# Optimization experiments

Measured on AMD Instinct MI355X. Metric: run time of the kernel, lower is better.

## Reference

```python
import jax, jax.numpy as jnp
import numpy as np

B, L, D_IN, D_H, D_OUT = 8, 1024, 1024, 1024, 1024


def setup_inputs() -> dict:
    key = jax.random.key(0)
    ks = jax.random.split(key, 9)
    s = 0.02  # weight scale to keep ReLU chain stable
    return {
        "leaves": jax.random.normal(ks[0], (B, L, D_IN), dtype=jnp.float32),
        "V_w": jax.random.normal(ks[1], (D_H, D_IN), dtype=jnp.float32) * s,
        "V_b": jax.random.normal(ks[2], (D_H,), dtype=jnp.float32) * s,
        "U_w": jax.random.normal(ks[3], (D_H, D_H), dtype=jnp.float32) * s,
        "U_b": jax.random.normal(ks[4], (D_H,), dtype=jnp.float32) * s,
        "W_w": jax.random.normal(ks[5], (D_H, D_H), dtype=jnp.float32) * s,
        "W_b": jax.random.normal(ks[6], (D_H,), dtype=jnp.float32) * s,
        "O_w": jax.random.normal(ks[7], (D_OUT, D_H), dtype=jnp.float32) * s,
        "O_b": jax.random.normal(ks[8], (D_OUT,), dtype=jnp.float32) * s,
    }


def reference(leaves, V_w, V_b, U_w, U_b, W_w, W_b, O_w, O_b):
    # Leaf encoding: h_leaf = relu(V(x))            [B, L, H]
    h = jax.nn.relu(jnp.einsum("bli,hi->blh", leaves, V_w) + V_b)
    # Depth-batched recursion over the complete binary tree:
    # combined = relu(U(left) + W(right)); log2(L) levels, node count halves.
    while h.shape[1] > 1:
        left, right = h[:, 0::2], h[:, 1::2]  # [B, n/2, H] each
        h = jax.nn.relu(
            jnp.einsum("bnh,gh->bng", left, U_w) + U_b
            + jnp.einsum("bnh,gh->bng", right, W_w) + W_b
        )
    root = h[:, 0]  # [B, H]
    logits = jnp.einsum("bh,oh->bo", root, O_w) + O_b
    return jax.nn.log_softmax(logits, axis=-1)
```

## Files before the change

### kernel.cpp

```cpp
#include <hip/hip_runtime.h>
#include <hip/hip_bf16.h>
#include <math.h>

typedef __bf16 bf16_t;
typedef __bf16 bf16x8 __attribute__((ext_vector_type(8)));
typedef __bf16 bf16x4 __attribute__((ext_vector_type(4)));
typedef float  f32x4  __attribute__((ext_vector_type(4)));

#define GLD_LDS16(g, l)                                                          \
  __builtin_amdgcn_global_load_lds((const __attribute__((address_space(1))) void*)(g), \
                                   (__attribute__((address_space(3))) void*)(l), 16, 0, 0)

__global__ __launch_bounds__(256) void k_cvt_bf16(const float* __restrict__ in,
                                                  bf16_t* __restrict__ out, int n4) {
  int i = blockIdx.x * 256 + threadIdx.x;
  if (i >= n4) return;
  float4 v = reinterpret_cast<const float4*>(in)[i];
  bf16x4 o;
  o[0] = (bf16_t)v.x; o[1] = (bf16_t)v.y; o[2] = (bf16_t)v.z; o[3] = (bf16_t)v.w;
  reinterpret_cast<bf16x4*>(out)[i] = o;
}

__global__ __launch_bounds__(256) void k_build_uw(const float* __restrict__ U,
                                                  const float* __restrict__ W,
                                                  const float* __restrict__ Ub,
                                                  const float* __restrict__ Wb,
                                                  bf16_t* __restrict__ UW,
                                                  float* __restrict__ buw) {
  int idx = blockIdx.x * 256 + threadIdx.x;
  int i = idx * 4;
  int g = i >> 11;
  int k = i & 2047;
  const float* src = (k < 1024) ? (U + g * 1024 + k) : (W + g * 1024 + (k - 1024));
  float4 v = *reinterpret_cast<const float4*>(src);
  bf16x4 o;
  o[0] = (bf16_t)v.x; o[1] = (bf16_t)v.y; o[2] = (bf16_t)v.z; o[3] = (bf16_t)v.w;
  reinterpret_cast<bf16x4*>(UW)[idx] = o;
  if (idx < 1024) buw[idx] = Ub[idx] + Wb[idx];
}

template <int TM, bool SPLIT>
__global__ __launch_bounds__(256) void k_gemm(const bf16_t* __restrict__ A,
                                              const bf16_t* __restrict__ Bw,
                                              const float* __restrict__ bias,
                                              bf16_t* __restrict__ C,
                                              float* __restrict__ P,
                                              int M, int K, int kchunk) {
  constexpr int N = 1024;
  constexpr int MI = TM / 32;
  __shared__ bf16_t As[3][TM * 32];
  __shared__ bf16_t Bs[3][128 * 32];

  const int tid = threadIdx.x;
  const int lane = tid & 63;
  const int wave = tid >> 6;
  const int wr = wave >> 1, wc = wave & 1;
  const int bm = blockIdx.x, bn = blockIdx.y, bz = blockIdx.z;
  const int kbase = bz * kchunk;

  const bf16_t* Abase = A + (size_t)bm * TM * K + kbase;
  const bf16_t* Bbase = Bw + (size_t)bn * 128 * K + kbase;

  f32x4 acc[MI][4] = {};
  const int rl = lane & 15, kq = lane >> 4;

  auto stage = [&](int buf, int ko) {
#pragma unroll
    for (int it = 0; it < TM / 64; ++it) {
      int c = tid + 256 * it;
      int r = c >> 2, kbp = c & 3;
      int kb = kbp ^ ((r >> 1) & 3);
      GLD_LDS16(Abase + (size_t)r * K + ko + kb * 8, &As[buf][c * 8]);
    }
#pragma unroll
    for (int it = 0; it < 2; ++it) {
      int c = tid + 256 * it;
      int r = c >> 2, kbp = c & 3;
      int kb = kbp ^ ((r >> 1) & 3);
      GLD_LDS16(Bbase + (size_t)r * K + ko + kb * 8, &Bs[buf][c * 8]);
    }
  };

  const int kiters = kchunk >> 5;
  stage(0, 0);
  stage(1, 32);

  int cur = 0;
  for (int t = 0; t < kiters; ++t) {
    if (t + 1 < kiters) {
      asm volatile("s_waitcnt vmcnt(3)" ::: "memory");
    } else {
      asm volatile("s_waitcnt vmcnt(0)" ::: "memory");
    }
    __builtin_amdgcn_s_barrier();
    __builtin_amdgcn_sched_barrier(0);
    if (t + 2 < kiters) {
      int b2 = cur + 2; if (b2 >= 3) b2 -= 3;
      stage(b2, (t + 2) * 32);
    }
    bf16x8 af[MI], bfr[4];
#pragma unroll
    for (int i = 0; i < MI; ++i) {
      int r = wr * (TM / 2) + i * 16 + rl;
      int kbp = kq ^ ((r >> 1) & 3);
      af[i] = *reinterpret_cast<const bf16x8*>(&As[cur][r * 32 + kbp * 8]);
    }
#pragma unroll
    for (int j = 0; j < 4; ++j) {
      int r = wc * 64 + j * 16 + rl;
      int kbp = kq ^ ((r >> 1) & 3);
      bfr[j] = *reinterpret_cast<const bf16x8*>(&Bs[cur][r * 32 + kbp * 8]);
    }
#pragma unroll
    for (int i = 0; i < MI; ++i)
#pragma unroll
      for (int j = 0; j < 4; ++j)
        acc[i][j] = __builtin_amdgcn_mfma_f32_16x16x32_bf16(af[i], bfr[j], acc[i][j], 0, 0, 0);
    if (++cur >= 3) cur = 0;
  }

  const int rq = lane >> 4, cl = lane & 15;
  if (SPLIT) {
    float* Pp = P + (size_t)bz * M * N;
#pragma unroll
    for (int i = 0; i < MI; ++i) {
#pragma unroll
      for (int j = 0; j < 4; ++j) {
        int grow = bm * TM + wr * (TM / 2) + i * 16 + rq * 4;
        int gcol = bn * 128 + wc * 64 + j * 16 + cl;
#pragma unroll
        for (int reg = 0; reg < 4; ++reg)
          Pp[(size_t)(grow + reg) * N + gcol] = acc[i][j][reg];
      }
    }
  } else {
#pragma unroll
    for (int j = 0; j < 4; ++j) {
      int gcol = bn * 128 + wc * 64 + j * 16 + cl;
      float bv = bias[gcol];
#pragma unroll
      for (int i = 0; i < MI; ++i) {
        int grow = bm * TM + wr * (TM / 2) + i * 16 + rq * 4;
#pragma unroll
        for (int reg = 0; reg < 4; ++reg) {
          float v = acc[i][j][reg] + bv;
          v = v > 0.0f ? v : 0.0f;
          C[(size_t)(grow + reg) * N + gcol] = (bf16_t)v;
        }
      }
    }
  }
}

__global__ __launch_bounds__(256) void k_reduce(const float* __restrict__ P,
                                                const float* __restrict__ bias,
                                                bf16_t* __restrict__ C, int M, int ks) {
  constexpr int N = 1024;
  int idx = blockIdx.x * 256 + threadIdx.x;
  int col = (idx * 4) & (N - 1);
  int row = (idx * 4) >> 10;
  float4 s = *reinterpret_cast<const float4*>(P + (size_t)row * N + col);
  for (int z = 1; z < ks; ++z) {
    float4 v = *reinterpret_cast<const float4*>(P + ((size_t)z * M + row) * N + col);
    s.x += v.x; s.y += v.y; s.z += v.z; s.w += v.w;
  }
  float4 b = *reinterpret_cast<const float4*>(bias + col);
  bf16x4 o;
  o[0] = (bf16_t)fmaxf(s.x + b.x, 0.0f);
  o[1] = (bf16_t)fmaxf(s.y + b.y, 0.0f);
  o[2] = (bf16_t)fmaxf(s.z + b.z, 0.0f);
  o[3] = (bf16_t)fmaxf(s.w + b.w, 0.0f);
  reinterpret_cast<bf16x4*>(C)[idx] = o;
}

__global__ __launch_bounds__(256) void k_tail(const bf16_t* __restrict__ A,
                                              const bf16_t* __restrict__ Bw,
                                              const float* __restrict__ bias,
                                              bf16_t* __restrict__ C, int M) {
  constexpr int N = 1024, K = 2048;
  const int lane = threadIdx.x & 63;
  const int gw = blockIdx.x * 4 + (threadIdx.x >> 6);
  const int n = gw & (N - 1);
  const int mbase = (gw >> 10) * 8;
  const int k0 = lane * 32;

  float bv[32];
  const bf16_t* bp = Bw + (size_t)n * K + k0;
#pragma unroll
  for (int q = 0; q < 4; ++q) {
    bf16x8 v = *reinterpret_cast<const bf16x8*>(bp + q * 8);
#pragma unroll
    for (int j = 0; j < 8; ++j) bv[q * 8 + j] = (float)v[j];
  }

  float acc[8];
#pragma unroll
  for (int m = 0; m < 8; ++m) {
    const bf16_t* ap = A + (size_t)(mbase + m) * K + k0;
    float s = 0.0f;
#pragma unroll
    for (int q = 0; q < 4; ++q) {
      bf16x8 v = *reinterpret_cast<const bf16x8*>(ap + q * 8);
#pragma unroll
      for (int j = 0; j < 8; ++j) s += (float)v[j] * bv[q * 8 + j];
    }
    acc[m] = s;
  }
#pragma unroll
  for (int m = 0; m < 8; ++m) {
    acc[m] += __shfl_xor(acc[m], 32, 64);
    acc[m] += __shfl_xor(acc[m], 16, 64);
    acc[m] += __shfl_xor(acc[m], 8, 64);
    acc[m] += __shfl_xor(acc[m], 4, 64);
    acc[m] += __shfl_xor(acc[m], 2, 64);
    acc[m] += __shfl_xor(acc[m], 1, 64);
  }
  if (lane < 8 && mbase + lane < M) {
    float v = acc[lane] + bias[n];
    v = v > 0.0f ? v : 0.0f;
    C[(size_t)(mbase + lane) * N + n] = (bf16_t)v;
  }
}

__global__ __launch_bounds__(256) void k_logits(const bf16_t* __restrict__ root,
                                                const bf16_t* __restrict__ Ow,
                                                const float* __restrict__ Ob,
                                                float* __restrict__ out) {
  int o = blockIdx.x * 256 + threadIdx.x;
  int b = blockIdx.y;
  const bf16_t* r = root + b * 1024;
  const bf16_t* w = Ow + (size_t)o * 1024;
  float s = 0.0f;
#pragma unroll 4
  for (int k = 0; k < 1024; k += 8) {
    bf16x8 rv = *reinterpret_cast<const bf16x8*>(r + k);
    bf16x8 wv = *reinterpret_cast<const bf16x8*>(w + k);
#pragma unroll
    for (int j = 0; j < 8; ++j) s += (float)rv[j] * (float)wv[j];
  }
  out[b * 1024 + o] = s + Ob[o];
}

__device__ inline float wave_max_f(float v) {
#pragma unroll
  for (int off = 32; off > 0; off >>= 1) v = fmaxf(v, __shfl_xor(v, off, 64));
  return v;
}
__device__ inline float wave_sum_f(float v) {
#pragma unroll
  for (int off = 32; off > 0; off >>= 1) v += __shfl_xor(v, off, 64);
  return v;
}

__global__ __launch_bounds__(256) void k_logsoftmax(const float* __restrict__ logits,
                                                    float* __restrict__ out) {
  int b = blockIdx.x;
  const float* x = logits + b * 1024;
  int tid = threadIdx.x;
  int wave = tid >> 6, lane = tid & 63;
  __shared__ float red[8];

  float m = -1e30f;
  for (int i = tid; i < 1024; i += 256) m = fmaxf(m, x[i]);
  m = wave_max_f(m);
  if (lane == 0) red[wave] = m;
  __syncthreads();
  if (tid == 0) red[4] = fmaxf(fmaxf(red[0], red[1]), fmaxf(red[2], red[3]));
  __syncthreads();
  m = red[4];

  float s = 0.0f;
  for (int i = tid; i < 1024; i += 256) s += expf(x[i] - m);
  s = wave_sum_f(s);
  if (lane == 0) red[wave] = s;
  __syncthreads();
  if (tid == 0) red[5] = logf(red[0] + red[1] + red[2] + red[3]);
  __syncthreads();
  float lse = m + red[5];
  for (int i = tid; i < 1024; i += 256) out[b * 1024 + i] = x[i] - lse;
}

extern "C" void kernel_launch(void* const* d_in, const int* in_sizes, int n_in,
                              void* d_out, int out_size, void* d_ws, size_t ws_size,
                              hipStream_t stream) {
  const float* leaves = (const float*)d_in[0];
  const float* V_w = (const float*)d_in[1];
  const float* V_b = (const float*)d_in[2];
  const float* U_w = (const float*)d_in[3];
  const float* U_b = (const float*)d_in[4];
  const float* W_w = (const float*)d_in[5];
  const float* W_b = (const float*)d_in[6];
  const float* O_w = (const float*)d_in[7];
  const float* O_b = (const float*)d_in[8];
  float* out = (float*)d_out;

  char* ws = (char*)d_ws;
  size_t off = 0;
  auto alloc = [&](size_t bytes) -> void* {
    off = (off + 255) & ~(size_t)255;
    void* p = ws + off;
    off += bytes;
    return p;
  };

  const size_t MB16 = (size_t)8192 * 1024 * 2;
  bf16_t* leaves_bf = (bf16_t*)alloc(MB16);
  bf16_t* Vw_bf = (bf16_t*)alloc((size_t)1024 * 1024 * 2);
  bf16_t* UW_bf = (bf16_t*)alloc((size_t)2 * 1024 * 1024 * 2);
  bf16_t* Ow_bf = (bf16_t*)alloc((size_t)1024 * 1024 * 2);
  float* buw = (float*)alloc(1024 * 4);
  bf16_t* hA = (bf16_t*)alloc(MB16);
  float* logits = (float*)alloc(8 * 1024 * 4);
  float* Pbuf = (float*)alloc((size_t)4 * 2048 * 1024 * 4);
  (void)ws_size; (void)in_sizes; (void)n_in; (void)out_size;

  k_cvt_bf16<<<(8 * 1024 * 1024 / 4) / 256, 256, 0, stream>>>(leaves, leaves_bf, 8 * 1024 * 1024 / 4);
  k_cvt_bf16<<<(1024 * 1024 / 4) / 256, 256, 0, stream>>>(V_w, Vw_bf, 1024 * 1024 / 4);
  k_cvt_bf16<<<(1024 * 1024 / 4) / 256, 256, 0, stream>>>(O_w, Ow_bf, 1024 * 1024 / 4);
  k_build_uw<<<2048, 256, 0, stream>>>(U_w, W_w, U_b, W_b, UW_bf, buw);

  k_gemm<64, false><<<dim3(128, 8), 256, 0, stream>>>(leaves_bf, Vw_bf, V_b, hA, nullptr,
                                                      8192, 1024, 1024);

  bf16_t* src = hA;
  bf16_t* dst = leaves_bf;
  auto swap = [&]() { bf16_t* t = src; src = dst; dst = t; };

  k_gemm<64, false><<<dim3(64, 8), 256, 0, stream>>>(src, UW_bf, buw, dst, nullptr,
                                                     4096, 2048, 2048);
  swap();
  k_gemm<64, true><<<dim3(32, 8, 2), 256, 0, stream>>>(src, UW_bf, nullptr, nullptr, Pbuf,
                                                       2048, 2048, 1024);
  k_reduce<<<2048 * 1024 / 4 / 256, 256, 0, stream>>>(Pbuf, buw, dst, 2048, 2);
  swap();
  k_gemm<64, true><<<dim3(16, 8, 4), 256, 0, stream>>>(src, UW_bf, nullptr, nullptr, Pbuf,
                                                       1024, 2048, 512);
  k_reduce<<<1024 * 1024 / 4 / 256, 256, 0, stream>>>(Pbuf, buw, dst, 1024, 4);
  swap();
  k_gemm<64, true><<<dim3(8, 8, 4), 256, 0, stream>>>(src, UW_bf, nullptr, nullptr, Pbuf,
                                                      512, 2048, 512);
  k_reduce<<<512 * 1024 / 4 / 256, 256, 0, stream>>>(Pbuf, buw, dst, 512, 4);
  swap();
  k_gemm<64, true><<<dim3(4, 8, 8), 256, 0, stream>>>(src, UW_bf, nullptr, nullptr, Pbuf,
                                                      256, 2048, 256);
  k_reduce<<<256 * 1024 / 4 / 256, 256, 0, stream>>>(Pbuf, buw, dst, 256, 8);
  swap();
  k_gemm<64, true><<<dim3(2, 8, 8), 256, 0, stream>>>(src, UW_bf, nullptr, nullptr, Pbuf,
                                                      128, 2048, 256);
  k_reduce<<<128 * 1024 / 4 / 256, 256, 0, stream>>>(Pbuf, buw, dst, 128, 8);
  swap();
  for (int M = 64; M >= 8; M >>= 1) {
    int blocks = (M / 8) * 1024 / 4;
    k_tail<<<blocks, 256, 0, stream>>>(src, UW_bf, buw, dst, M);
    swap();
  }

  k_logits<<<dim3(4, 8), 256, 0, stream>>>(src, Ow_bf, O_b, logits);
  k_logsoftmax<<<8, 256, 0, stream>>>(logits, out);
}
```

Measured before the change: 233.7 us.

## Replace split-K GEMM plus reduce with narrower-N tiles; fuse conversion kernels

Merges the four fp32-to-bf16 conversion launches into one grid-stride kernel. For tree levels M=2048..128, drops the split-K GEMM that wrote fp32 partials and the separate reduce kernel. These levels now use a single full-K GEMM with a 64x64 tile, which doubles the N-dimension block count and fuses bias+ReLU into the epilogue. This removes the partial-sum round trip through memory and one launch per level. The cost is fewer blocks on the small levels, with each block running the full K=2048 loop serially, so the late levels may lose parallelism.

```diff
diff --git a/kernel.cpp b/kernel.cpp
--- a/kernel.cpp
+++ b/kernel.cpp
@@ -11,57 +11,69 @@
   __builtin_amdgcn_global_load_lds((const __attribute__((address_space(1))) void*)(g), \
                                    (__attribute__((address_space(3))) void*)(l), 16, 0, 0)
 
-__global__ __launch_bounds__(256) void k_cvt_bf16(const float* __restrict__ in,
-                                                  bf16_t* __restrict__ out, int n4) {
-  int i = blockIdx.x * 256 + threadIdx.x;
-  if (i >= n4) return;
-  float4 v = reinterpret_cast<const float4*>(in)[i];
-  bf16x4 o;
-  o[0] = (bf16_t)v.x; o[1] = (bf16_t)v.y; o[2] = (bf16_t)v.z; o[3] = (bf16_t)v.w;
-  reinterpret_cast<bf16x4*>(out)[i] = o;
-}
-
-__global__ __launch_bounds__(256) void k_build_uw(const float* __restrict__ U,
-                                                  const float* __restrict__ W,
-                                                  const float* __restrict__ Ub,
-                                                  const float* __restrict__ Wb,
-                                                  bf16_t* __restrict__ UW,
-                                                  float* __restrict__ buw) {
-  int idx = blockIdx.x * 256 + threadIdx.x;
-  int i = idx * 4;
-  int g = i >> 11;
-  int k = i & 2047;
-  const float* src = (k < 1024) ? (U + g * 1024 + k) : (W + g * 1024 + (k - 1024));
-  float4 v = *reinterpret_cast<const float4*>(src);
-  bf16x4 o;
-  o[0] = (bf16_t)v.x; o[1] = (bf16_t)v.y; o[2] = (bf16_t)v.z; o[3] = (bf16_t)v.w;
-  reinterpret_cast<bf16x4*>(UW)[idx] = o;
-  if (idx < 1024) buw[idx] = Ub[idx] + Wb[idx];
-}
-
-template <int TM, bool SPLIT>
-__global__ __launch_bounds__(256) void k_gemm(const bf16_t* __restrict__ A,
-                                              const bf16_t* __restrict__ Bw,
-                                              const float* __restrict__ bias,
-                                              bf16_t* __restrict__ C,
-                                              float* __restrict__ P,
-                                              int M, int K, int kchunk) {
-  constexpr int N = 1024;
+__global__ __launch_bounds__(256) void k_cvt_all(const float* __restrict__ leaves,
+                                                 const float* __restrict__ V_w,
+                                                 const float* __restrict__ O_w,
+                                                 const float* __restrict__ U_w,
+                                                 const float* __restrict__ W_w,
+                                                 const float* __restrict__ U_b,
+                                                 const float* __restrict__ W_b,
+                                                 bf16_t* __restrict__ leaves_bf,
+                                                 bf16_t* __restrict__ Vw_bf,
+                                                 bf16_t* __restrict__ Ow_bf,
+                                                 bf16_t* __restrict__ UW_bf,
+                                                 float* __restrict__ buw) {
+  const int gtid = blockIdx.x * 256 + threadIdx.x;
+  const int G = gridDim.x * 256;
+  for (int i = gtid; i < 2097152; i += G) {
+    float4 v = reinterpret_cast<const float4*>(leaves)[i];
+    bf16x4 o; o[0] = (bf16_t)v.x; o[1] = (bf16_t)v.y; o[2] = (bf16_t)v.z; o[3] = (bf16_t)v.w;
+    reinterpret_cast<bf16x4*>(leaves_bf)[i] = o;
+  }
+  for (int i = gtid; i < 262144; i += G) {
+    float4 v = reinterpret_cast<const float4*>(V_w)[i];
+    bf16x4 o; o[0] = (bf16_t)v.x; o[1] = (bf16_t)v.y; o[2] = (bf16_t)v.z; o[3] = (bf16_t)v.w;
+    reinterpret_cast<bf16x4*>(Vw_bf)[i] = o;
+  }
+  for (int i = gtid; i < 262144; i += G) {
+    float4 v = reinterpret_cast<const float4*>(O_w)[i];
+    bf16x4 o; o[0] = (bf16_t)v.x; o[1] = (bf16_t)v.y; o[2] = (bf16_t)v.z; o[3] = (bf16_t)v.w;
+    reinterpret_cast<bf16x4*>(Ow_bf)[i] = o;
+  }
+  for (int idx = gtid; idx < 524288; idx += G) {
+    int i = idx * 4;
+    int g = i >> 11;
+    int k = i & 2047;
+    const float* src = (k < 1024) ? (U_w + g * 1024 + k) : (W_w + g * 1024 + (k - 1024));
+    float4 v = *reinterpret_cast<const float4*>(src);
+    bf16x4 o; o[0] = (bf16_t)v.x; o[1] = (bf16_t)v.y; o[2] = (bf16_t)v.z; o[3] = (bf16_t)v.w;
+    reinterpret_cast<bf16x4*>(UW_bf)[idx] = o;
+  }
+  if (gtid < 1024) buw[gtid] = U_b[gtid] + W_b[gtid];
+}
+
+template <int TM, int TN>
+__global__ __launch_bounds__(256, 4) void k_gemm(const bf16_t* __restrict__ A,
+                                                 const bf16_t* __restrict__ Bw,
+                                                 const float* __restrict__ bias,
+                                                 bf16_t* __restrict__ C,
+                                                 int K) {
   constexpr int MI = TM / 32;
+  constexpr int NJ = TN / 32;
+  constexpr int VM = TM / 64 + TN / 64;
   __shared__ bf16_t As[3][TM * 32];
-  __shared__ bf16_t Bs[3][128 * 32];
+  __shared__ bf16_t Bs[3][TN * 32];
 
   const int tid = threadIdx.x;
   const int lane = tid & 63;
   const int wave = tid >> 6;
   const int wr = wave >> 1, wc = wave & 1;
-  const int bm = blockIdx.x, bn = blockIdx.y, bz = blockIdx.z;
-  const int kbase = bz * kchunk;
-
-  const bf16_t* Abase = A + (size_t)bm * TM * K + kbase;
-  const bf16_t* Bbase = Bw + (size_t)bn * 128 * K + kbase;
-
-  f32x4 acc[MI][4] = {};
+  const int bm = blockIdx.x, bn = blockIdx.y;
+
+  const bf16_t* Abase = A + (size_t)bm * TM * K;
+  const bf16_t* Bbase = Bw + (size_t)bn * TN * K;
+
+  f32x4 acc[MI][NJ] = {};
   const int rl = lane & 15, kq = lane >> 4;
 
   auto stage = [&](int buf, int ko) {
@@ -73,7 +85,7 @@
       GLD_LDS16(Abase + (size_t)r * K + ko + kb * 8, &As[buf][c * 8]);
     }
 #pragma unroll
-    for (int it = 0; it < 2; ++it) {
+    for (int it = 0; it < TN / 64; ++it) {
       int c = tid + 256 * it;
       int r = c >> 2, kbp = c & 3;
       int kb = kbp ^ ((r >> 1) & 3);
@@ -81,24 +93,21 @@
     }
   };
 
-  const int kiters = kchunk >> 5;
+  const int kiters = K >> 5;
   stage(0, 0);
   stage(1, 32);
 
   int cur = 0;
   for (int t = 0; t < kiters; ++t) {
-    if (t + 1 < kiters) {
-      asm volatile("s_waitcnt vmcnt(3)" ::: "memory");
-    } else {
-      asm volatile("s_waitcnt vmcnt(0)" ::: "memory");
-    }
+    if (t + 1 < kiters) asm volatile("s_waitcnt vmcnt(%0)" :: "i"(VM) : "memory");
+    else                asm volatile("s_waitcnt vmcnt(0)" ::: "memory");
     __builtin_amdgcn_s_barrier();
     __builtin_amdgcn_sched_barrier(0);
     if (t + 2 < kiters) {
       int b2 = cur + 2; if (b2 >= 3) b2 -= 3;
       stage(b2, (t + 2) * 32);
     }
-    bf16x8 af[MI], bfr[4];
+    bf16x8 af[MI], bfr[NJ];
 #pragma unroll
     for (int i = 0; i < MI; ++i) {
       int r = wr * (TM / 2) + i * 16 + rl;
@@ -106,71 +115,35 @@
       af[i] = *reinterpret_cast<const bf16x8*>(&As[cur][r * 32 + kbp * 8]);
     }
 #pragma unroll
-    for (int j = 0; j < 4; ++j) {
-      int r = wc * 64 + j * 16 + rl;
+    for (int j = 0; j < NJ; ++j) {
+      int r = wc * (TN / 2) + j * 16 + rl;
       int kbp = kq ^ ((r >> 1) & 3);
       bfr[j] = *reinterpret_cast<const bf16x8*>(&Bs[cur][r * 32 + kbp * 8]);
     }
 #pragma unroll
     for (int i = 0; i < MI; ++i)
 #pragma unroll
-      for (int j = 0; j < 4; ++j)
+      for (int j = 0; j < NJ; ++j)
         acc[i][j] = __builtin_amdgcn_mfma_f32_16x16x32_bf16(af[i], bfr[j], acc[i][j], 0, 0, 0);
     if (++cur >= 3) cur = 0;
   }
 
   const int rq = lane >> 4, cl = lane & 15;
-  if (SPLIT) {
-    float* Pp = P + (size_t)bz * M * N;
+#pragma unroll
+  for (int j = 0; j < NJ; ++j) {
+    int gcol = bn * TN + wc * (TN / 2) + j * 16 + cl;
+    float bv = bias[gcol];
 #pragma unroll
     for (int i = 0; i < MI; ++i) {
-#pragma unroll
-      for (int j = 0; j < 4; ++j) {
-        int grow = bm * TM + wr * (TM / 2) + i * 16 + rq * 4;
-        int gcol = bn * 128 + wc * 64 + j * 16 + cl;
-#pragma unroll
-        for (int reg = 0; reg < 4; ++reg)
-          Pp[(size_t)(grow + reg) * N + gcol] = acc[i][j][reg];
+      int grow = bm * TM + wr * (TM / 2) + i * 16 + rq * 4;
+#pragma unroll
+      for (int reg = 0; reg < 4; ++reg) {
+        float v = acc[i][j][reg] + bv;
+        v = v > 0.0f ? v : 0.0f;
+        C[(size_t)(grow + reg) * 1024 + gcol] = (bf16_t)v;
       }
     }
-  } else {
-#pragma unroll
-    for (int j = 0; j < 4; ++j) {
-      int gcol = bn * 128 + wc * 64 + j * 16 + cl;
-      float bv = bias[gcol];
-#pragma unroll
-      for (int i = 0; i < MI; ++i) {
-        int grow = bm * TM + wr * (TM / 2) + i * 16 + rq * 4;
-#pragma unroll
-        for (int reg = 0; reg < 4; ++reg) {
-          float v = acc[i][j][reg] + bv;
-          v = v > 0.0f ? v : 0.0f;
-          C[(size_t)(grow + reg) * N + gcol] = (bf16_t)v;
-        }
-      }
-    }
-  }
-}
-
-__global__ __launch_bounds__(256) void k_reduce(const float* __restrict__ P,
-                                                const float* __restrict__ bias,
-                                                bf16_t* __restrict__ C, int M, int ks) {
-  constexpr int N = 1024;
-  int idx = blockIdx.x * 256 + threadIdx.x;
-  int col = (idx * 4) & (N - 1);
-  int row = (idx * 4) >> 10;
-  float4 s = *reinterpret_cast<const float4*>(P + (size_t)row * N + col);
-  for (int z = 1; z < ks; ++z) {
-    float4 v = *reinterpret_cast<const float4*>(P + ((size_t)z * M + row) * N + col);
-    s.x += v.x; s.y += v.y; s.z += v.z; s.w += v.w;
-  }
-  float4 b = *reinterpret_cast<const float4*>(bias + col);
-  bf16x4 o;
-  o[0] = (bf16_t)fmaxf(s.x + b.x, 0.0f);
-  o[1] = (bf16_t)fmaxf(s.y + b.y, 0.0f);
-  o[2] = (bf16_t)fmaxf(s.z + b.z, 0.0f);
-  o[3] = (bf16_t)fmaxf(s.w + b.w, 0.0f);
-  reinterpret_cast<bf16x4*>(C)[idx] = o;
+  }
 }
 
 __global__ __launch_bounds__(256) void k_tail(const bf16_t* __restrict__ A,
@@ -208,12 +181,8 @@
   }
 #pragma unroll
   for (int m = 0; m < 8; ++m) {
-    acc[m] += __shfl_xor(acc[m], 32, 64);
-    acc[m] += __shfl_xor(acc[m], 16, 64);
-    acc[m] += __shfl_xor(acc[m], 8, 64);
-    acc[m] += __shfl_xor(acc[m], 4, 64);
-    acc[m] += __shfl_xor(acc[m], 2, 64);
-    acc[m] += __shfl_xor(acc[m], 1, 64);
+#pragma unroll
+    for (int off = 32; off >= 1; off >>= 1) acc[m] += __shfl_xor(acc[m], off, 64);
   }
   if (lane < 8 && mbase + lane < M) {
     float v = acc[lane] + bias[n];
@@ -241,17 +210,6 @@
   out[b * 1024 + o] = s + Ob[o];
 }
 
-__device__ inline float wave_max_f(float v) {
-#pragma unroll
-  for (int off = 32; off > 0; off >>= 1) v = fmaxf(v, __shfl_xor(v, off, 64));
-  return v;
-}
-__device__ inline float wave_sum_f(float v) {
-#pragma unroll
-  for (int off = 32; off > 0; off >>= 1) v += __shfl_xor(v, off, 64);
-  return v;
-}
-
 __global__ __launch_bounds__(256) void k_logsoftmax(const float* __restrict__ logits,
                                                     float* __restrict__ out) {
   int b = blockIdx.x;
@@ -262,21 +220,18 @@
 
   float m = -1e30f;
   for (int i = tid; i < 1024; i += 256) m = fmaxf(m, x[i]);
-  m = wave_max_f(m);
+#pragma unroll
+  for (int off = 32; off >= 1; off >>= 1) m = fmaxf(m, __shfl_xor(m, off, 64));
   if (lane == 0) red[wave] = m;
   __syncthreads();
-  if (tid == 0) red[4] = fmaxf(fmaxf(red[0], red[1]), fmaxf(red[2], red[3]));
-  __syncthreads();
-  m = red[4];
-
+  m = fmaxf(fmaxf(red[0], red[1]), fmaxf(red[2], red[3]));
   float s = 0.0f;
   for (int i = tid; i < 1024; i += 256) s += expf(x[i] - m);
-  s = wave_sum_f(s);
+#pragma unroll
+  for (int off = 32; off >= 1; off >>= 1) s += __shfl_xor(s, off, 64);
   if (lane == 0) red[wave] = s;
   __syncthreads();
-  if (tid == 0) red[5] = logf(red[0] + red[1] + red[2] + red[3]);
-  __syncthreads();
-  float lse = m + red[5];
+  float lse = m + logf(red[0] + red[1] + red[2] + red[3]);
   for (int i = tid; i < 1024; i += 256) out[b * 1024 + i] = x[i] - lse;
 }
 
@@ -311,44 +266,23 @@
   float* buw = (float*)alloc(1024 * 4);
   bf16_t* hA = (bf16_t*)alloc(MB16);
   float* logits = (float*)alloc(8 * 1024 * 4);
-  float* Pbuf = (float*)alloc((size_t)4 * 2048 * 1024 * 4);
   (void)ws_size; (void)in_sizes; (void)n_in; (void)out_size;
 
-  k_cvt_bf16<<<(8 * 1024 * 1024 / 4) / 256, 256, 0, stream>>>(leaves, leaves_bf, 8 * 1024 * 1024 / 4);
-  k_cvt_bf16<<<(1024 * 1024 / 4) / 256, 256, 0, stream>>>(V_w, Vw_bf, 1024 * 1024 / 4);
-  k_cvt_bf16<<<(1024 * 1024 / 4) / 256, 256, 0, stream>>>(O_w, Ow_bf, 1024 * 1024 / 4);
-  k_build_uw<<<2048, 256, 0, stream>>>(U_w, W_w, U_b, W_b, UW_bf, buw);
-
-  k_gemm<64, false><<<dim3(128, 8), 256, 0, stream>>>(leaves_bf, Vw_bf, V_b, hA, nullptr,
-                                                      8192, 1024, 1024);
+  k_cvt_all<<<2048, 256, 0, stream>>>(leaves, V_w, O_w, U_w, W_w, U_b, W_b,
+                                      leaves_bf, Vw_bf, Ow_bf, UW_bf, buw);
+
+  k_gemm<64, 128><<<dim3(128, 8), 256, 0, stream>>>(leaves_bf, Vw_bf, V_b, hA, 1024);
 
   bf16_t* src = hA;
   bf16_t* dst = leaves_bf;
   auto swap = [&]() { bf16_t* t = src; src = dst; dst = t; };
 
-  k_gemm<64, false><<<dim3(64, 8), 256, 0, stream>>>(src, UW_bf, buw, dst, nullptr,
-                                                     4096, 2048, 2048);
+  k_gemm<64, 128><<<dim3(64, 8), 256, 0, stream>>>(src, UW_bf, buw, dst, 2048);
   swap();
-  k_gemm<64, true><<<dim3(32, 8, 2), 256, 0, stream>>>(src, UW_bf, nullptr, nullptr, Pbuf,
-                                                       2048, 2048, 1024);
-  k_reduce<<<2048 * 1024 / 4 / 256, 256, 0, stream>>>(Pbuf, buw, dst, 2048, 2);
-  swap();
-  k_gemm<64, true><<<dim3(16, 8, 4), 256, 0, stream>>>(src, UW_bf, nullptr, nullptr, Pbuf,
-                                                       1024, 2048, 512);
-  k_reduce<<<1024 * 1024 / 4 / 256, 256, 0, stream>>>(Pbuf, buw, dst, 1024, 4);
-  swap();
-  k_gemm<64, true><<<dim3(8, 8, 4), 256, 0, stream>>>(src, UW_bf, nullptr, nullptr, Pbuf,
-                                                      512, 2048, 512);
-  k_reduce<<<512 * 1024 / 4 / 256, 256, 0, stream>>>(Pbuf, buw, dst, 512, 4);
-  swap();
-  k_gemm<64, true><<<dim3(4, 8, 8), 256, 0, stream>>>(src, UW_bf, nullptr, nullptr, Pbuf,
-                                                      256, 2048, 256);
-  k_reduce<<<256 * 1024 / 4 / 256, 256, 0, stream>>>(Pbuf, buw, dst, 256, 8);
-  swap();
-  k_gemm<64, true><<<dim3(2, 8, 8), 256, 0, stream>>>(src, UW_bf, nullptr, nullptr, Pbuf,
-                                                      128, 2048, 256);
-  k_reduce<<<128 * 1024 / 4 / 256, 256, 0, stream>>>(Pbuf, buw, dst, 128, 8);
-  swap();
+  for (int M = 2048; M >= 128; M >>= 1) {
+    k_gemm<64, 64><<<dim3(M / 64, 16), 256, 0, stream>>>(src, UW_bf, buw, dst, 2048);
+    swap();
+  }
   for (int M = 64; M >= 8; M >>= 1) {
     int blocks = (M / 8) * 1024 / 4;
     k_tail<<<blocks, 256, 0, stream>>>(src, UW_bf, buw, dst, M);
```

After: 274.3 us. 1.17x slower.
